# Performance work log

Measured on AMD Instinct MI355X. Metric: run time of the kernel, lower is better.

Reference implementation:

```python
import jax, jax.numpy as jnp
import numpy as np


def setup_inputs() -> dict:
    key = jax.random.key(0)
    k1, k2 = jax.random.split(key)
    B, F, E, D = 16384, 50, 64, 128
    inputs = jax.random.normal(k1, (B, F, E), dtype=jnp.float32)
    Theta = jax.random.normal(k2, (D, F), dtype=jnp.float32)
    return {"inputs": inputs, "Theta": Theta}


def reference(inputs, Theta):
    # Original loop: for each d, proj_d = sum_f Theta[d,f] * inputs[:,f,:]  -> [B, E]
    # then L_p[:, d] = sum_e proj_d**2.
    # Fused: single contraction over fields, then squared reduction over embed dim.
    proj = jnp.einsum("df,bfe->bde", Theta, inputs)  # [B, D, E]
    L_p = jnp.sum(proj * proj, axis=-1)  # [B, D]
    return L_p
```

## Files before the change

### kernel.cpp

```cpp
#include <hip/hip_runtime.h>


#define NB 8
constexpr int kF = 50;
constexpr int kE = 64;
constexpr int kD = 128;
constexpr int kFE = kF * kE;

typedef __attribute__((ext_vector_type(8))) short short8;
typedef __attribute__((ext_vector_type(4))) float f32x4;

__device__ __forceinline__ short f2bf(float f) {
  unsigned u = __float_as_uint(f);
  u += 0x7FFFu + ((u >> 16) & 1u);
  return (short)(u >> 16);
}

__global__ __launch_bounds__(256, 3) void ip_kernel(
    const float* __restrict__ X, const float* __restrict__ Th,
    float* __restrict__ out) {
  const int tid  = threadIdx.x;
  const int wid  = tid >> 6;
  const int lane = tid & 63;
  const int q    = lane >> 4;
  const int m16  = lane & 15;

  short8 th[2][2];
  const int d0 = wid * 32;
#pragma unroll
  for (int dt = 0; dt < 2; ++dt) {
    const float* trow = Th + (size_t)(d0 + dt * 16 + m16) * kF;
#pragma unroll
    for (int ks = 0; ks < 2; ++ks) {
      short8 v;
#pragma unroll
      for (int j = 0; j < 8; ++j) {
        const int k = ks * 32 + q * 8 + j;
        const float f = (k < kF) ? trow[k] : 0.0f;
        v[j] = f2bf(f);
      }
      th[dt][ks] = v;
    }
  }

  const int b0 = blockIdx.x * NB;
  for (int ib = 0; ib < NB; ++ib) {
    const int b = b0 + ib;
    const float* xb = X + (size_t)b * kFE + m16;

    f32x4 acc[4][2];
#pragma unroll
    for (int et = 0; et < 4; ++et)
#pragma unroll
      for (int dt = 0; dt < 2; ++dt)
        acc[et][dt] = (f32x4){0.f, 0.f, 0.f, 0.f};

    float xbuf[2][16];
#pragma unroll
    for (int i = 0; i < 16; ++i) {
      const int k = (i >> 3) * 32 + q * 8 + (i & 7);
      xbuf[0][i] = (k < kF) ? xb[k * kE] : 0.0f;
    }

#pragma unroll
    for (int et = 0; et < 4; ++et) {
      if (et < 3) {
#pragma unroll
        for (int i = 0; i < 16; ++i) {
          const int k = (i >> 3) * 32 + q * 8 + (i & 7);
          xbuf[(et + 1) & 1][i] = (k < kF) ? xb[k * kE + (et + 1) * 16] : 0.0f;
        }
      }
      short8 af[2];
#pragma unroll
      for (int ks = 0; ks < 2; ++ks) {
        short8 v;
#pragma unroll
        for (int j = 0; j < 8; ++j) v[j] = f2bf(xbuf[et & 1][ks * 8 + j]);
        af[ks] = v;
      }
#pragma unroll
      for (int dt = 0; dt < 2; ++dt) {
        acc[et][dt] = __builtin_amdgcn_mfma_f32_16x16x32_bf16(af[0], th[dt][0], acc[et][dt], 0, 0, 0);
        acc[et][dt] = __builtin_amdgcn_mfma_f32_16x16x32_bf16(af[1], th[dt][1], acc[et][dt], 0, 0, 0);
      }
    }

    float* orow = out + (size_t)b * kD + d0;
#pragma unroll
    for (int dt = 0; dt < 2; ++dt) {
      float s = 0.0f;
#pragma unroll
      for (int et = 0; et < 4; ++et)
#pragma unroll
        for (int r = 0; r < 4; ++r) {
          const float p = acc[et][dt][r];
          s = fmaf(p, p, s);
        }
      s += __shfl_xor(s, 16, 64);
      s += __shfl_xor(s, 32, 64);
      if (lane < 16) orow[dt * 16 + lane] = s;
    }
  }
}

extern "C" void kernel_launch(void* const* d_in, const int* in_sizes, int n_in,
                              void* d_out, int out_size, void* d_ws, size_t ws_size,
                              hipStream_t stream) {
  const float* X  = (const float*)d_in[0];
  const float* Th = (const float*)d_in[1];
  float* out = (float*)d_out;
  ip_kernel<<<dim3(16384 / NB), dim3(256), 0, stream>>>(X, Th, out);
}
```

Baseline: 322.0 us.

## Stage batch rows into LDS as bf16 once, shared across waves

```diff
diff --git a/kernel.cpp b/kernel.cpp
--- a/kernel.cpp
+++ b/kernel.cpp
@@ -2,12 +2,14 @@
 
 
 #define NB 8
-constexpr int kF = 50;
-constexpr int kE = 64;
-constexpr int kD = 128;
+constexpr int kF  = 50;
+constexpr int kE  = 64;
+constexpr int kD  = 128;
 constexpr int kFE = kF * kE;
+constexpr int FS  = 72;
 
 typedef __attribute__((ext_vector_type(8))) short short8;
+typedef __attribute__((ext_vector_type(4))) short bf16x4;
 typedef __attribute__((ext_vector_type(4))) float f32x4;
 
 __device__ __forceinline__ short f2bf(float f) {
@@ -16,14 +18,23 @@
   return (short)(u >> 16);
 }
 
-__global__ __launch_bounds__(256, 3) void ip_kernel(
+__global__ __launch_bounds__(256, 4) void ip_kernel(
     const float* __restrict__ X, const float* __restrict__ Th,
     float* __restrict__ out) {
+  __shared__ __align__(16) short lds[2][kE * FS];
+
   const int tid  = threadIdx.x;
   const int wid  = tid >> 6;
   const int lane = tid & 63;
   const int q    = lane >> 4;
   const int m16  = lane & 15;
+  const int se   = lane;
+
+  for (int i = tid; i < kE * 12 * 2; i += 256) {
+    const int buf = (i >= kE * 12) ? 1 : 0;
+    const int r = i - buf * kE * 12;
+    lds[buf][(r / 12) * FS + 52 + (r % 12)] = 0;
+  }
 
   short8 th[2][2];
   const int d0 = wid * 32;
@@ -36,57 +47,59 @@
 #pragma unroll
       for (int j = 0; j < 8; ++j) {
         const int k = ks * 32 + q * 8 + j;
-        const float f = (k < kF) ? trow[k] : 0.0f;
-        v[j] = f2bf(f);
+        v[j] = (k < kF) ? f2bf(trow[k]) : (short)0;
       }
       th[dt][ks] = v;
     }
   }
 
+  auto stage = [&](int buf, int b) {
+    const float* xb = X + (size_t)b * kFE + se;
+    short* row = &lds[buf][se * FS];
+#pragma unroll
+    for (int p = 0; p < 3; ++p) {
+      bf16x4 w;
+#pragma unroll
+      for (int j = 0; j < 4; ++j) w[j] = f2bf(xb[(16 * p + 4 * wid + j) * kE]);
+      *reinterpret_cast<bf16x4*>(&row[16 * p + 4 * wid]) = w;
+    }
+    if (wid == 0) {
+      bf16x4 w;
+      w[0] = f2bf(xb[48 * kE]);
+      w[1] = f2bf(xb[49 * kE]);
+      w[2] = 0; w[3] = 0;
+      *reinterpret_cast<bf16x4*>(&row[48]) = w;
+    }
+  };
+
   const int b0 = blockIdx.x * NB;
+  stage(0, b0);
+  __syncthreads();
+
   for (int ib = 0; ib < NB; ++ib) {
+    const int cur = ib & 1;
     const int b = b0 + ib;
-    const float* xb = X + (size_t)b * kFE + m16;
+    if (ib + 1 < NB) stage(cur ^ 1, b + 1);
 
+    const short* L = &lds[cur][m16 * FS + q * 8];
     f32x4 acc[4][2];
 #pragma unroll
     for (int et = 0; et < 4; ++et)
 #pragma unroll
-      for (int dt = 0; dt < 2; ++dt)
-        acc[et][dt] = (f32x4){0.f, 0.f, 0.f, 0.f};
-
-    float xbuf[2][16];
-#pragma unroll
-    for (int i = 0; i < 16; ++i) {
-      const int k = (i >> 3) * 32 + q * 8 + (i & 7);
-      xbuf[0][i] = (k < kF) ? xb[k * kE] : 0.0f;
-    }
+      for (int dt = 0; dt < 2; ++dt) acc[et][dt] = (f32x4){0.f, 0.f, 0.f, 0.f};
 
 #pragma unroll
     for (int et = 0; et < 4; ++et) {
-      if (et < 3) {
-#pragma unroll
-        for (int i = 0; i < 16; ++i) {
-          const int k = (i >> 3) * 32 + q * 8 + (i & 7);
-          xbuf[(et + 1) & 1][i] = (k < kF) ? xb[k * kE + (et + 1) * 16] : 0.0f;
-        }
-      }
-      short8 af[2];
-#pragma unroll
-      for (int ks = 0; ks < 2; ++ks) {
-        short8 v;
-#pragma unroll
-        for (int j = 0; j < 8; ++j) v[j] = f2bf(xbuf[et & 1][ks * 8 + j]);
-        af[ks] = v;
-      }
+      const short8 a0 = *reinterpret_cast<const short8*>(&L[et * 16 * FS]);
+      const short8 a1 = *reinterpret_cast<const short8*>(&L[et * 16 * FS + 32]);
 #pragma unroll
       for (int dt = 0; dt < 2; ++dt) {
-        acc[et][dt] = __builtin_amdgcn_mfma_f32_16x16x32_bf16(af[0], th[dt][0], acc[et][dt], 0, 0, 0);
-        acc[et][dt] = __builtin_amdgcn_mfma_f32_16x16x32_bf16(af[1], th[dt][1], acc[et][dt], 0, 0, 0);
+        acc[et][dt] = __builtin_amdgcn_mfma_f32_16x16x32_bf16(a0, th[dt][0], acc[et][dt], 0, 0, 0);
+        acc[et][dt] = __builtin_amdgcn_mfma_f32_16x16x32_bf16(a1, th[dt][1], acc[et][dt], 0, 0, 0);
       }
     }
 
-    float* orow = out + (size_t)b * kD + d0;
+    float sv[2];
 #pragma unroll
     for (int dt = 0; dt < 2; ++dt) {
       float s = 0.0f;
@@ -99,8 +112,11 @@
         }
       s += __shfl_xor(s, 16, 64);
       s += __shfl_xor(s, 32, 64);
-      if (lane < 16) orow[dt * 16 + lane] = s;
+      sv[dt] = s;
     }
+    if (lane < 32) out[(size_t)b * kD + d0 + lane] = (lane < 16) ? sv[0] : sv[1];
+
+    __syncthreads();
   }
 }
 
```

New measurement: 294.1 us. -8.7%, faster.
